# Kernel tuning notes

Measured on AMD Instinct MI355X. Metric: run time of the kernel, lower is better.

## Reference

```python
import jax, jax.numpy as jnp
import numpy as np

N_NODES = 50000
N_EDGES = 800000
D = 128
K_HOPS = 2  # ConvLayer k=2 -> k+1=3 accumulated terms


def conv_layer(feat, src, dst, W, b):
    # DGL-style symmetric-norm GCN hop accumulation (method='sum', relu)
    n = feat.shape[0]
    ones = jnp.ones(src.shape[0], dtype=feat.dtype)
    deg = jax.ops.segment_sum(ones, src, num_segments=n)  # out-degrees
    norm = jnp.clip(deg, 1.0, None) ** -0.5  # [N]
    norm = norm[:, None]
    rst = feat @ W + b
    for _ in range(K_HOPS):
        feat = feat * norm
        # update_all(copy_u, sum): gather src features, scatter-sum to dst
        feat = jax.ops.segment_sum(feat[src], dst, num_segments=n)
        feat = feat * norm
        rst = rst + feat @ W + b  # original code reuses weights[0] each hop
    return jax.nn.relu(rst)


def setup_inputs() -> dict:
    key = jax.random.key(0)
    ks = jax.random.split(key, 6)
    xavier = (6.0 / (D + D)) ** 0.5
    feat = jax.random.normal(ks[0], (N_NODES, D), dtype=jnp.float32)
    src = jax.random.randint(ks[1], (N_EDGES,), 0, N_NODES, dtype=jnp.int32)
    dst = jax.random.randint(ks[2], (N_EDGES,), 0, N_NODES, dtype=jnp.int32)
    W1 = jax.random.uniform(ks[3], (D, D), jnp.float32, -xavier, xavier)
    W2 = jax.random.uniform(ks[4], (D, D), jnp.float32, -xavier, xavier)
    b1 = jnp.zeros((D,), jnp.float32)
    b2 = jnp.zeros((D,), jnp.float32)
    return {"feat": feat, "W1": W1, "b1": b1, "W2": W2, "b2": b2,
            "src": src, "dst": dst}


def reference(feat, W1, b1, W2, b2, src, dst):
    # GraphEmbbeding: stacked ConvLayers (num_layers=2)
    h = conv_layer(feat, src, dst, W1, b1)
    h = conv_layer(h, src, dst, W2, b2)
    return h
```

## Files before the change

kernel.cpp:

```cpp
#include <hip/hip_runtime.h>

#define N_NODES 50000
#define N_EDGES 800000
#define D 128
#define NSB ((N_NODES + 255) / 256)
#define NCH 64
#define EPC (N_EDGES / NCH)
#define NR 4
#define RNG (N_NODES / NR)

typedef unsigned short ushort_t;
typedef unsigned int uint_t;
typedef short s16x8 __attribute__((ext_vector_type(8)));
typedef float f32x4 __attribute__((ext_vector_type(4)));

__device__ __forceinline__ float bf2f(ushort_t u) {
    uint_t x = ((uint_t)u) << 16;
    return __builtin_bit_cast(float, x);
}
__device__ __forceinline__ ushort_t f2bf(float f) {
    uint_t u = __builtin_bit_cast(uint_t, f);
    uint_t r = (u + 0x7FFFu + ((u >> 16) & 1u)) >> 16;
    return (ushort_t)r;
}

__global__ __launch_bounds__(256) void kb_hist(const int* __restrict__ src,
        const int* __restrict__ dst, uint_t* __restrict__ hist) {
    __shared__ uint_t h[RNG];
    int chunk = blockIdx.x, range = blockIdx.y;
    int base = range * RNG;
    int t = threadIdx.x;
    for (int i = t; i < RNG; i += 256) h[i] = 0;
    __syncthreads();
    int e0 = chunk * EPC;
    for (int e = e0 + t; e < e0 + EPC; e += 256) {
        unsigned su = (unsigned)(src[e] - base);
        unsigned du = (unsigned)(dst[e] - base);
        if (su < RNG) atomicAdd(&h[su], 1u << 16);
        if (du < RNG) atomicAdd(&h[du], 1u);
    }
    __syncthreads();
    uint_t* oh = hist + (size_t)chunk * N_NODES + base;
    for (int i = t; i < RNG; i += 256) oh[i] = h[i];
}

__global__ __launch_bounds__(256) void kb_reduce(uint_t* __restrict__ hist,
        int* __restrict__ off, int* __restrict__ bsum,
        float* __restrict__ norm, float* __restrict__ rnorm) {
    __shared__ int sh[256];
    int t = threadIdx.x;
    int n = blockIdx.x * 256 + t;
    int run = 0, od = 0;
    if (n < N_NODES) {
#pragma unroll 8
        for (int c = 0; c < NCH; ++c) {
            size_t idx = (size_t)c * N_NODES + n;
            uint_t v = hist[idx];
            hist[idx] = (uint_t)run;
            run += (int)(v & 0xFFFFu);
            od  += (int)(v >> 16);
        }
        float dg = fmaxf((float)od, 1.0f);
        norm[n]  = 1.0f / sqrtf(dg);
        rnorm[n] = sqrtf(dg);
    }
    sh[t] = run;
    __syncthreads();
    for (int d = 1; d < 256; d <<= 1) {
        int x = sh[t];
        int y = (t >= d) ? sh[t - d] : 0;
        __syncthreads();
        sh[t] = x + y;
        __syncthreads();
    }
    if (n < N_NODES) off[n] = sh[t] - run;
    if (t == 255) bsum[blockIdx.x] = sh[255];
}

__global__ void k_scanB(const int* __restrict__ bsum, int* __restrict__ bbase,
                        int* __restrict__ off) {
    __shared__ int sh[256];
    int t = threadIdx.x;
    int v = (t < NSB) ? bsum[t] : 0;
    sh[t] = v;
    __syncthreads();
    for (int d = 1; d < 256; d <<= 1) {
        int x = sh[t];
        int y = (t >= d) ? sh[t - d] : 0;
        __syncthreads();
        sh[t] = x + y;
        __syncthreads();
    }
    if (t < NSB) bbase[t] = sh[t] - v;
    if (t == 255) off[N_NODES] = sh[255];
}

__global__ void k_scanC(int* __restrict__ off, const int* __restrict__ bbase) {
    int i = blockIdx.x * 256 + threadIdx.x;
    if (i < N_NODES) off[i] += bbase[blockIdx.x];
}

__global__ __launch_bounds__(256) void kb_scatter(const int* __restrict__ src,
        const int* __restrict__ dst, const int* __restrict__ off,
        const uint_t* __restrict__ hist, int* __restrict__ csrc) {
    __shared__ int slot[RNG];
    int chunk = blockIdx.x, range = blockIdx.y;
    int base = range * RNG;
    int t = threadIdx.x;
    const uint_t* hb = hist + (size_t)chunk * N_NODES + base;
    for (int i = t; i < RNG; i += 256) slot[i] = off[base + i] + (int)hb[i];
    __syncthreads();
    int e0 = chunk * EPC;
    for (int e = e0 + t; e < e0 + EPC; e += 256) {
        unsigned du = (unsigned)(dst[e] - base);
        if (du < RNG) {
            int p = atomicAdd(&slot[du], 1);
            csrc[p] = src[e];
        }
    }
}

__global__ void k_prepw(const float* __restrict__ W1, const float* __restrict__ W2,
                        ushort_t* __restrict__ Wt1, ushort_t* __restrict__ Wt2) {
    int i = blockIdx.x * 256 + threadIdx.x;
    const float* W = blockIdx.y ? W2 : W1;
    ushort_t* Wt = blockIdx.y ? Wt2 : Wt1;
    if (i < D * D) {
        int col = i >> 7, k = i & 127;
        Wt[i] = f2bf(W[(size_t)k * D + col]);
    }
}

__global__ void k_init(const float* __restrict__ X, const float* __restrict__ norm,
                       ushort_t* __restrict__ A) {
    int i = blockIdx.x * blockDim.x + threadIdx.x;
    const int total = N_NODES * (D / 4);
    if (i < total) {
        int row = i >> 5;
        float4 v = ((const float4*)X)[i];
        float nm = norm[row];
        ushort4 a = {f2bf(v.x * nm), f2bf(v.y * nm), f2bf(v.z * nm), f2bf(v.w * nm)};
        ((ushort4*)A)[i] = a;
    }
}

__global__ __launch_bounds__(256, 2) void k_prop(const ushort_t* __restrict__ Ain,
                       const int* __restrict__ off, const int* __restrict__ csrc,
                       const float* __restrict__ norm,
                       ushort_t* __restrict__ Aout, int mode) {
    int w = blockIdx.x * 16 + (threadIdx.x >> 4);
    if (w >= N_NODES) return;
    int li = threadIdx.x & 15;
    int s0 = off[w], s1 = off[w + 1];
    float a0=0.f,a1=0.f,a2=0.f,a3=0.f,a4=0.f,a5=0.f,a6=0.f,a7=0.f;
    const s16x8* A8 = (const s16x8*)Ain;
    int j = s0;
    for (; j + 16 <= s1; j += 16) {
        int idx[16];
#pragma unroll
        for (int k = 0; k < 16; ++k) idx[k] = csrc[j + k];
        s16x8 v[16];
#pragma unroll
        for (int k = 0; k < 16; ++k) v[k] = A8[(size_t)idx[k] * 16 + li];
#pragma unroll
        for (int k = 0; k < 16; ++k) {
            a0 += bf2f((ushort_t)v[k][0]); a1 += bf2f((ushort_t)v[k][1]);
            a2 += bf2f((ushort_t)v[k][2]); a3 += bf2f((ushort_t)v[k][3]);
            a4 += bf2f((ushort_t)v[k][4]); a5 += bf2f((ushort_t)v[k][5]);
            a6 += bf2f((ushort_t)v[k][6]); a7 += bf2f((ushort_t)v[k][7]);
        }
    }
    if (j < s1) {
        int e1 = s1 - 1;
        for (; j < s1; j += 8) {
            int idx[8]; float wk[8];
#pragma unroll
            for (int k = 0; k < 8; ++k) {
                int jj = j + k;
                idx[k] = csrc[jj < s1 ? jj : e1];
                wk[k] = (jj < s1) ? 1.f : 0.f;
            }
            s16x8 v[8];
#pragma unroll
            for (int k = 0; k < 8; ++k) v[k] = A8[(size_t)idx[k] * 16 + li];
#pragma unroll
            for (int k = 0; k < 8; ++k) {
                a0 = fmaf(wk[k], bf2f((ushort_t)v[k][0]), a0);
                a1 = fmaf(wk[k], bf2f((ushort_t)v[k][1]), a1);
                a2 = fmaf(wk[k], bf2f((ushort_t)v[k][2]), a2);
                a3 = fmaf(wk[k], bf2f((ushort_t)v[k][3]), a3);
                a4 = fmaf(wk[k], bf2f((ushort_t)v[k][4]), a4);
                a5 = fmaf(wk[k], bf2f((ushort_t)v[k][5]), a5);
                a6 = fmaf(wk[k], bf2f((ushort_t)v[k][6]), a6);
                a7 = fmaf(wk[k], bf2f((ushort_t)v[k][7]), a7);
            }
        }
    }
    float nm = norm[w];
    float f = mode ? nm : nm * nm;
    s16x8 o;
    o[0] = (short)f2bf(a0 * f); o[1] = (short)f2bf(a1 * f);
    o[2] = (short)f2bf(a2 * f); o[3] = (short)f2bf(a3 * f);
    o[4] = (short)f2bf(a4 * f); o[5] = (short)f2bf(a5 * f);
    o[6] = (short)f2bf(a6 * f); o[7] = (short)f2bf(a7 * f);
    ((s16x8*)Aout)[(size_t)w * 16 + li] = o;
}

__global__ __launch_bounds__(256) void k_gemm_relu(const float* __restrict__ X0f,
        const ushort_t* __restrict__ X0h,
        const ushort_t* __restrict__ A1, const ushort_t* __restrict__ X2,
        const float* __restrict__ rnorm,
        const ushort_t* __restrict__ Wt, const float* __restrict__ bias,
        float* __restrict__ outf, ushort_t* __restrict__ Hbf,
        ushort_t* __restrict__ Anext,
        const float* __restrict__ norm, float bscale) {
    __shared__ ushort_t Xs[64 * D];
    __shared__ ushort_t Ws[D * D];
    int t = threadIdx.x;
    int row0 = blockIdx.x * 64;
    const s16x8* Wg = (const s16x8*)Wt;
    s16x8* Ws8 = (s16x8*)Ws;
    for (int i = t; i < D * 16; i += 256) {
        int col = i >> 4, c = i & 15;
        Ws8[(col << 4) | (c ^ (col & 7))] = Wg[i];
    }
    s16x8* Xs8 = (s16x8*)Xs;
    for (int i = t; i < 64 * 16; i += 256) {
        int r = i >> 4, c = i & 15;
        int gr = row0 + r;
        s16x8 ov;
        if (gr < N_NODES) {
            size_t b4 = (size_t)gr * 32 + c * 2;
            float x[8];
            if (X0f) {
                float4 x0a = ((const float4*)X0f)[b4], x0b = ((const float4*)X0f)[b4 + 1];
                x[0]=x0a.x; x[1]=x0a.y; x[2]=x0a.z; x[3]=x0a.w;
                x[4]=x0b.x; x[5]=x0b.y; x[6]=x0b.z; x[7]=x0b.w;
            } else {
                ushort4 h0 = ((const ushort4*)X0h)[b4], h1 = ((const ushort4*)X0h)[b4 + 1];
                x[0]=bf2f(h0.x); x[1]=bf2f(h0.y); x[2]=bf2f(h0.z); x[3]=bf2f(h0.w);
                x[4]=bf2f(h1.x); x[5]=bf2f(h1.y); x[6]=bf2f(h1.z); x[7]=bf2f(h1.w);
            }
            ushort4 p0 = ((const ushort4*)A1)[b4], p1 = ((const ushort4*)A1)[b4 + 1];
            ushort4 q0 = ((const ushort4*)X2)[b4], q1 = ((const ushort4*)X2)[b4 + 1];
            float rn = rnorm[gr];
            ov[0] = (short)f2bf(x[0] + bf2f(p0.x) * rn + bf2f(q0.x));
            ov[1] = (short)f2bf(x[1] + bf2f(p0.y) * rn + bf2f(q0.y));
            ov[2] = (short)f2bf(x[2] + bf2f(p0.z) * rn + bf2f(q0.z));
            ov[3] = (short)f2bf(x[3] + bf2f(p0.w) * rn + bf2f(q0.w));
            ov[4] = (short)f2bf(x[4] + bf2f(p1.x) * rn + bf2f(q1.x));
            ov[5] = (short)f2bf(x[5] + bf2f(p1.y) * rn + bf2f(q1.y));
            ov[6] = (short)f2bf(x[6] + bf2f(p1.z) * rn + bf2f(q1.z));
            ov[7] = (short)f2bf(x[7] + bf2f(p1.w) * rn + bf2f(q1.w));
        } else {
            ov = (s16x8)0;
        }
        Xs8[(r << 4) | (c ^ (r & 7))] = ov;
    }
    __syncthreads();
    int wid = t >> 6, l = t & 63;
    int lrow = l & 15, lk = l >> 4;
    f32x4 acc[8];
#pragma unroll
    for (int nt = 0; nt < 8; ++nt) acc[nt] = (f32x4){0.f, 0.f, 0.f, 0.f};
    const s16x8* Xr = (const s16x8*)Xs;
    const s16x8* Wr = (const s16x8*)Ws;
#pragma unroll
    for (int ks = 0; ks < 4; ++ks) {
        int kc = ks * 4 + lk;
        int ar = wid * 16 + lrow;
        s16x8 a = Xr[(ar << 4) | (kc ^ (ar & 7))];
#pragma unroll
        for (int nt = 0; nt < 8; ++nt) {
            int bc = nt * 16 + lrow;
            s16x8 b = Wr[(bc << 4) | (kc ^ (bc & 7))];
            acc[nt] = __builtin_amdgcn_mfma_f32_16x16x32_bf16(a, b, acc[nt], 0, 0, 0);
        }
    }
    int rbase = row0 + wid * 16 + lk * 4;
#pragma unroll
    for (int nt = 0; nt < 8; ++nt) {
        int C = nt * 16 + lrow;
        float bv = bias[C] * bscale;
#pragma unroll
        for (int r = 0; r < 4; ++r) {
            int R = rbase + r;
            if (R < N_NODES) {
                float o = fmaxf(acc[nt][r] + bv, 0.f);
                size_t oi = (size_t)R * D + C;
                if (outf) outf[oi] = o;
                if (Hbf) Hbf[oi] = f2bf(o);
                if (Anext) Anext[oi] = f2bf(o * norm[R]);
            }
        }
    }
}

extern "C" void kernel_launch(void* const* d_in, const int* in_sizes, int n_in,
                              void* d_out, int out_size, void* d_ws, size_t ws_size,
                              hipStream_t stream) {
    const float* feat = (const float*)d_in[0];
    const float* W1   = (const float*)d_in[1];
    const float* b1   = (const float*)d_in[2];
    const float* W2   = (const float*)d_in[3];
    const float* b2   = (const float*)d_in[4];
    const int*   src  = (const int*)d_in[5];
    const int*   dst  = (const int*)d_in[6];
    float* out = (float*)d_out;

    char* ws = (char*)d_ws;
    size_t o = 0;
    auto alloc = [&](size_t bytes) {
        void* p = ws + o;
        o += (bytes + 1023) & ~(size_t)1023;
        return p;
    };
    uint_t*   hist  = (uint_t*)alloc((size_t)NCH * N_NODES * 4);
    float*    norm  = (float*)alloc(N_NODES * 4);
    float*    rnorm = (float*)alloc(N_NODES * 4);
    int*      off   = (int*)alloc((N_NODES + 1) * 4);
    int*      bsum  = (int*)alloc(NSB * 4);
    int*      bbase = (int*)alloc(NSB * 4);
    int*      csrc  = (int*)alloc((size_t)N_EDGES * 4);
    ushort_t* bufA  = (ushort_t*)alloc((size_t)N_NODES * D * 2);
    ushort_t* bufB  = (ushort_t*)alloc((size_t)N_NODES * D * 2);
    ushort_t* bufC  = (ushort_t*)alloc((size_t)N_NODES * D * 2);
    ushort_t* bufD  = (ushort_t*)alloc((size_t)N_NODES * D * 2);
    ushort_t* Wt1   = (ushort_t*)alloc((size_t)D * D * 2);
    ushort_t* Wt2   = (ushort_t*)alloc((size_t)D * D * 2);
    (void)ws_size; (void)in_sizes; (void)n_in; (void)out_size;

    kb_hist<<<dim3(NCH, NR), 256, 0, stream>>>(src, dst, hist);
    kb_reduce<<<NSB, 256, 0, stream>>>(hist, off, bsum, norm, rnorm);
    k_scanB<<<1, 256, 0, stream>>>(bsum, bbase, off);
    k_scanC<<<NSB, 256, 0, stream>>>(off, bbase);
    kb_scatter<<<dim3(NCH, NR), 256, 0, stream>>>(src, dst, off, hist, csrc);
    k_prepw<<<dim3((D * D + 255) / 256, 2), 256, 0, stream>>>(W1, W2, Wt1, Wt2);

    const int init_blocks = (N_NODES * 32 + 255) / 256;
    const int prop_blocks = (N_NODES + 15) / 16;
    const int gemm_blocks = (N_NODES + 63) / 64;

    k_init<<<init_blocks, 256, 0, stream>>>(feat, norm, bufA);
    k_prop<<<prop_blocks, 256, 0, stream>>>(bufA, off, csrc, norm, bufB, 0);
    k_prop<<<prop_blocks, 256, 0, stream>>>(bufB, off, csrc, norm, bufC, 1);
    k_gemm_relu<<<gemm_blocks, 256, 0, stream>>>(feat, nullptr, bufB, bufC, rnorm,
                                                 Wt1, b1, nullptr, bufD, bufA, norm, 3.0f);

    k_prop<<<prop_blocks, 256, 0, stream>>>(bufA, off, csrc, norm, bufB, 0);
    k_prop<<<prop_blocks, 256, 0, stream>>>(bufB, off, csrc, norm, bufC, 1);
    k_gemm_relu<<<gemm_blocks, 256, 0, stream>>>(nullptr, bufD, bufB, bufC, rnorm,
                                                 Wt2, b2, out, nullptr, nullptr, norm, 3.0f);
}
```

Before: 236.4 us.

## Pack two node counters per word and split CSR histograms by array

The CSR-build histogram now packs two nodes' 16-bit counts into each 32-bit shared-memory word, so one block covers all nodes instead of four node ranges. Source and destination histograms are built by separate blocks, and each block reads only one edge array. The chunk count doubles, and the reduce, scan and scatter kernels are adapted to the paired layout. This cuts repeated edge-array reads across range blocks. In exchange each block needs about 100KB of LDS, which limits occupancy, and the 16-bit prefix fields would overflow on very high in-degree.

```diff
diff --git a/kernel.cpp b/kernel.cpp
--- a/kernel.cpp
+++ b/kernel.cpp
@@ -1,13 +1,12 @@
 #include <hip/hip_runtime.h>
 
 #define N_NODES 50000
+#define NP (N_NODES / 2)
 #define N_EDGES 800000
 #define D 128
-#define NSB ((N_NODES + 255) / 256)
-#define NCH 64
+#define NCH 128
 #define EPC (N_EDGES / NCH)
-#define NR 4
-#define RNG (N_NODES / NR)
+#define NRB ((NP + 255) / 256)
 
 typedef unsigned short ushort_t;
 typedef unsigned int uint_t;
@@ -25,46 +24,53 @@
 }
 
 __global__ __launch_bounds__(256) void kb_hist(const int* __restrict__ src,
-        const int* __restrict__ dst, uint_t* __restrict__ hist) {
-    __shared__ uint_t h[RNG];
-    int chunk = blockIdx.x, range = blockIdx.y;
-    int base = range * RNG;
-    int t = threadIdx.x;
-    for (int i = t; i < RNG; i += 256) h[i] = 0;
+        const int* __restrict__ dst, uint_t* __restrict__ dhist,
+        uint_t* __restrict__ shist) {
+    __shared__ uint_t h[NP];
+    int chunk = blockIdx.x;
+    const int* arr = blockIdx.y ? src : dst;
+    uint_t* out = (blockIdx.y ? shist : dhist) + (size_t)chunk * NP;
+    int t = threadIdx.x;
+    for (int i = t; i < NP; i += 256) h[i] = 0;
     __syncthreads();
     int e0 = chunk * EPC;
     for (int e = e0 + t; e < e0 + EPC; e += 256) {
-        unsigned su = (unsigned)(src[e] - base);
-        unsigned du = (unsigned)(dst[e] - base);
-        if (su < RNG) atomicAdd(&h[su], 1u << 16);
-        if (du < RNG) atomicAdd(&h[du], 1u);
-    }
-    __syncthreads();
-    uint_t* oh = hist + (size_t)chunk * N_NODES + base;
-    for (int i = t; i < RNG; i += 256) oh[i] = h[i];
-}
-
-__global__ __launch_bounds__(256) void kb_reduce(uint_t* __restrict__ hist,
+        int n = arr[e];
+        atomicAdd(&h[n >> 1], 1u << ((n & 1) * 16));
+    }
+    __syncthreads();
+    for (int i = t; i < NP; i += 256) out[i] = h[i];
+}
+
+__global__ __launch_bounds__(256) void kb_reduce(uint_t* __restrict__ dhist,
+        const uint_t* __restrict__ shist,
         int* __restrict__ off, int* __restrict__ bsum,
         float* __restrict__ norm, float* __restrict__ rnorm) {
     __shared__ int sh[256];
     int t = threadIdx.x;
-    int n = blockIdx.x * 256 + t;
-    int run = 0, od = 0;
-    if (n < N_NODES) {
+    int p = blockIdx.x * 256 + t;
+    int run0 = 0, run1 = 0, od0 = 0, od1 = 0;
+    if (p < NP) {
 #pragma unroll 8
         for (int c = 0; c < NCH; ++c) {
-            size_t idx = (size_t)c * N_NODES + n;
-            uint_t v = hist[idx];
-            hist[idx] = (uint_t)run;
-            run += (int)(v & 0xFFFFu);
-            od  += (int)(v >> 16);
-        }
-        float dg = fmaxf((float)od, 1.0f);
-        norm[n]  = 1.0f / sqrtf(dg);
-        rnorm[n] = sqrtf(dg);
-    }
-    sh[t] = run;
+            size_t idx = (size_t)c * NP + p;
+            uint_t v = dhist[idx];
+            dhist[idx] = (uint_t)(run0 | (run1 << 16));
+            run0 += (int)(v & 0xFFFFu);
+            run1 += (int)(v >> 16);
+            uint_t s = shist[idx];
+            od0 += (int)(s & 0xFFFFu);
+            od1 += (int)(s >> 16);
+        }
+        float dg0 = fmaxf((float)od0, 1.0f);
+        float dg1 = fmaxf((float)od1, 1.0f);
+        norm[2 * p]      = 1.0f / sqrtf(dg0);
+        rnorm[2 * p]     = sqrtf(dg0);
+        norm[2 * p + 1]  = 1.0f / sqrtf(dg1);
+        rnorm[2 * p + 1] = sqrtf(dg1);
+    }
+    int tot = run0 + run1;
+    sh[t] = tot;
     __syncthreads();
     for (int d = 1; d < 256; d <<= 1) {
         int x = sh[t];
@@ -73,7 +79,11 @@
         sh[t] = x + y;
         __syncthreads();
     }
-    if (n < N_NODES) off[n] = sh[t] - run;
+    if (p < NP) {
+        int base = sh[t] - tot;
+        off[2 * p]     = base;
+        off[2 * p + 1] = base + run0;
+    }
     if (t == 255) bsum[blockIdx.x] = sh[255];
 }
 
@@ -81,7 +91,7 @@
                         int* __restrict__ off) {
     __shared__ int sh[256];
     int t = threadIdx.x;
-    int v = (t < NSB) ? bsum[t] : 0;
+    int v = (t < NRB) ? bsum[t] : 0;
     sh[t] = v;
     __syncthreads();
     for (int d = 1; d < 256; d <<= 1) {
@@ -91,29 +101,33 @@
         sh[t] = x + y;
         __syncthreads();
     }
-    if (t < NSB) bbase[t] = sh[t] - v;
+    if (t < NRB) bbase[t] = sh[t] - v;
     if (t == 255) off[N_NODES] = sh[255];
 }
 
 __global__ void k_scanC(int* __restrict__ off, const int* __restrict__ bbase) {
     int i = blockIdx.x * 256 + threadIdx.x;
-    if (i < N_NODES) off[i] += bbase[blockIdx.x];
+    if (i < N_NODES) off[i] += bbase[i >> 9];
 }
 
 __global__ __launch_bounds__(256) void kb_scatter(const int* __restrict__ src,
         const int* __restrict__ dst, const int* __restrict__ off,
-        const uint_t* __restrict__ hist, int* __restrict__ csrc) {
-    __shared__ int slot[RNG];
+        const uint_t* __restrict__ dhist, int* __restrict__ csrc) {
+    __shared__ int slot[NP];
     int chunk = blockIdx.x, range = blockIdx.y;
-    int base = range * RNG;
-    int t = threadIdx.x;
-    const uint_t* hb = hist + (size_t)chunk * N_NODES + base;
-    for (int i = t; i < RNG; i += 256) slot[i] = off[base + i] + (int)hb[i];
+    int base = range * NP;
+    int t = threadIdx.x;
+    const uint_t* hb = dhist + (size_t)chunk * NP + range * (NP / 2);
+    for (int i = t; i < NP; i += 256) {
+        uint_t cb = hb[i >> 1];
+        int c16 = (int)((cb >> ((i & 1) * 16)) & 0xFFFFu);
+        slot[i] = off[base + i] + c16;
+    }
     __syncthreads();
     int e0 = chunk * EPC;
     for (int e = e0 + t; e < e0 + EPC; e += 256) {
         unsigned du = (unsigned)(dst[e] - base);
-        if (du < RNG) {
+        if (du < (unsigned)NP) {
             int p = atomicAdd(&slot[du], 1);
             csrc[p] = src[e];
         }
@@ -315,12 +329,13 @@
         o += (bytes + 1023) & ~(size_t)1023;
         return p;
     };
-    uint_t*   hist  = (uint_t*)alloc((size_t)NCH * N_NODES * 4);
+    uint_t*   dhist = (uint_t*)alloc((size_t)NCH * NP * 4);
+    uint_t*   shist = (uint_t*)alloc((size_t)NCH * NP * 4);
     float*    norm  = (float*)alloc(N_NODES * 4);
     float*    rnorm = (float*)alloc(N_NODES * 4);
     int*      off   = (int*)alloc((N_NODES + 1) * 4);
-    int*      bsum  = (int*)alloc(NSB * 4);
-    int*      bbase = (int*)alloc(NSB * 4);
+    int*      bsum  = (int*)alloc(NRB * 4);
+    int*      bbase = (int*)alloc(NRB * 4);
     int*      csrc  = (int*)alloc((size_t)N_EDGES * 4);
     ushort_t* bufA  = (ushort_t*)alloc((size_t)N_NODES * D * 2);
     ushort_t* bufB  = (ushort_t*)alloc((size_t)N_NODES * D * 2);
@@ -330,11 +345,11 @@
     ushort_t* Wt2   = (ushort_t*)alloc((size_t)D * D * 2);
     (void)ws_size; (void)in_sizes; (void)n_in; (void)out_size;
 
-    kb_hist<<<dim3(NCH, NR), 256, 0, stream>>>(src, dst, hist);
-    kb_reduce<<<NSB, 256, 0, stream>>>(hist, off, bsum, norm, rnorm);
+    kb_hist<<<dim3(NCH, 2), 256, 0, stream>>>(src, dst, dhist, shist);
+    kb_reduce<<<NRB, 256, 0, stream>>>(dhist, shist, off, bsum, norm, rnorm);
     k_scanB<<<1, 256, 0, stream>>>(bsum, bbase, off);
-    k_scanC<<<NSB, 256, 0, stream>>>(off, bbase);
-    kb_scatter<<<dim3(NCH, NR), 256, 0, stream>>>(src, dst, off, hist, csrc);
+    k_scanC<<<(N_NODES + 255) / 256, 256, 0, stream>>>(off, bbase);
+    kb_scatter<<<dim3(NCH, 2), 256, 0, stream>>>(src, dst, off, dhist, csrc);
     k_prepw<<<dim3((D * D + 255) / 256, 2), 256, 0, stream>>>(W1, W2, Wt1, Wt2);
 
     const int init_blocks = (N_NODES * 32 + 255) / 256;
```

Measured after the change: 229.5 us. -2.9%, faster.
